# Performance work log

Hardware: AMD Instinct MI355X
Metric: run time of the kernel (lower is better)

The kernel has to match this reference:

```python
import jax, jax.numpy as jnp
import numpy as np

D_MODEL = 1024
N_HEADS = 16
D_HEAD = D_MODEL // N_HEADS
LSR_RANK = 32
B, T = 2, 2048


def setup_inputs() -> dict:
    key = jax.random.key(0)
    ks = jax.random.split(key, 12)
    s = 1.0 / np.sqrt(D_MODEL)
    return {
        "x": jax.random.normal(ks[0], (B, T, D_MODEL), dtype=jnp.float32),
        "Wq": jax.random.normal(ks[1], (D_MODEL, D_MODEL), dtype=jnp.float32) * s,
        "bq": jnp.zeros((D_MODEL,), dtype=jnp.float32),
        "Wk": jax.random.normal(ks[2], (D_MODEL, D_MODEL), dtype=jnp.float32) * s,
        "bk": jnp.zeros((D_MODEL,), dtype=jnp.float32),
        "Wv": jax.random.normal(ks[3], (D_MODEL, D_MODEL), dtype=jnp.float32) * s,
        "bv": jnp.zeros((D_MODEL,), dtype=jnp.float32),
        "Wo": jax.random.normal(ks[4], (D_MODEL, D_MODEL), dtype=jnp.float32) * s,
        "bo": jnp.zeros((D_MODEL,), dtype=jnp.float32),
        "Wq_lsr": jax.random.normal(ks[5], (N_HEADS, D_HEAD, LSR_RANK), dtype=jnp.float32),
        "Wk_lsr": jax.random.normal(ks[6], (N_HEADS, D_HEAD, LSR_RANK), dtype=jnp.float32),
    }


def reference(x, Wq, bq, Wk, bk, Wv, bv, Wo, bo, Wq_lsr, Wk_lsr):
    Bn, Tn, dm = x.shape
    H, Dh, R = Wq_lsr.shape
    # q/k/v projections, split into heads: (B, H, T, Dh)
    def split_heads(y):
        return y.reshape(Bn, Tn, H, Dh).transpose(0, 2, 1, 3)
    q = split_heads(x @ Wq + bq)
    k = split_heads(x @ Wk + bk)
    v = split_heads(x @ Wv + bv)
    # low-rank projected scores: (Q Wq_lsr)(K Wk_lsr)^T / sqrt(R)
    q_lr = jnp.einsum('bhtd,hdr->bhtr', q, Wq_lsr)
    k_lr = jnp.einsum('bhtd,hdr->bhtr', k, Wk_lsr)
    scale = 1.0 / jnp.sqrt(jnp.float32(R))
    scores = jnp.einsum('bhir,bhjr->bhij', q_lr, k_lr) * scale
    # causal mask
    causal = jnp.tril(jnp.ones((Tn, Tn), dtype=bool))
    scores = jnp.where(causal[None, None], scores, -jnp.inf)
    attn = jax.nn.softmax(scores, axis=-1)
    out = jnp.einsum('bhij,bhjd->bhid', attn, v)  # (B, H, T, Dh)
    out = out.transpose(0, 2, 1, 3).reshape(Bn, Tn, dm)
    return out @ Wo + bo
```

## Files before the change

kernel.cpp:

```cpp
#include <hip/hip_runtime.h>
#include <math.h>

#define D_MODEL 1024
#define N_HEADS 16
#define D_HEAD  64
#define LSR_RANK 32
#define BATCH 2
#define SEQ 2048
#define M_TOT (BATCH*SEQ)

typedef __attribute__((ext_vector_type(8))) short short8v;
typedef __attribute__((ext_vector_type(4))) short short4v;
typedef __attribute__((ext_vector_type(4))) float f32x4;

static __device__ __forceinline__ ushort bfhi(float f) {
    union { float f; unsigned u; } c; c.f = f;
    return (ushort)(c.u >> 16);
}
static __device__ __forceinline__ float bff(ushort h) {
    union { unsigned u; float f; } c; c.u = ((unsigned)h) << 16;
    return c.f;
}
static __device__ __forceinline__ ushort f2bf_rn(float f) {
    union { float f; unsigned u; } c; c.f = f;
    unsigned r = c.u + 0x7FFF + ((c.u >> 16) & 1);
    return (ushort)(r >> 16);
}
static __device__ __forceinline__ void split8(const float4 a, const float4 b,
                                              short8v& h, short8v& l) {
    ushort h0 = bfhi(a.x), h1 = bfhi(a.y), h2 = bfhi(a.z), h3 = bfhi(a.w);
    ushort h4 = bfhi(b.x), h5 = bfhi(b.y), h6 = bfhi(b.z), h7 = bfhi(b.w);
    h[0] = (short)h0; h[1] = (short)h1; h[2] = (short)h2; h[3] = (short)h3;
    h[4] = (short)h4; h[5] = (short)h5; h[6] = (short)h6; h[7] = (short)h7;
    l[0] = (short)bfhi(a.x - bff(h0)); l[1] = (short)bfhi(a.y - bff(h1));
    l[2] = (short)bfhi(a.z - bff(h2)); l[3] = (short)bfhi(a.w - bff(h3));
    l[4] = (short)bfhi(b.x - bff(h4)); l[5] = (short)bfhi(b.y - bff(h5));
    l[6] = (short)bfhi(b.z - bff(h6)); l[7] = (short)bfhi(b.w - bff(h7));
}
static __device__ __forceinline__ void trunc8(const float4 a, const float4 b,
                                              short8v& h) {
    h[0] = (short)bfhi(a.x); h[1] = (short)bfhi(a.y);
    h[2] = (short)bfhi(a.z); h[3] = (short)bfhi(a.w);
    h[4] = (short)bfhi(b.x); h[5] = (short)bfhi(b.y);
    h[6] = (short)bfhi(b.z); h[7] = (short)bfhi(b.w);
}

__global__ __launch_bounds__(256) void eff_weight2(
    const float* __restrict__ Wq, const float* __restrict__ Wq_lsr,
    const float* __restrict__ Wk, const float* __restrict__ Wk_lsr,
    float* __restrict__ Weff_tmp)
{
    const int z = blockIdx.y;
    const float* W    = z ? Wk : Wq;
    const float* Wlsr = z ? Wk_lsr : Wq_lsr;
    const int base = z << 9;
    int idx = blockIdx.x * 256 + threadIdx.x;
    int k = idx >> 9;
    int c = idx & 511;
    int h = c >> 5;
    int r = c & 31;
    const float* wrow = W + (size_t)k * D_MODEL + h * D_HEAD;
    const float* lsr  = Wlsr + (size_t)h * D_HEAD * LSR_RANK + r;
    float acc = 0.f;
    #pragma unroll
    for (int d = 0; d < D_HEAD; ++d)
        acc = fmaf(wrow[d], lsr[d * LSR_RANK], acc);
    Weff_tmp[(size_t)k * 1024 + base + c] = acc;
}

__global__ __launch_bounds__(256) void eff_bias_kernel(
    const float* __restrict__ bq, const float* __restrict__ Wq_lsr,
    const float* __restrict__ bk, const float* __restrict__ Wk_lsr,
    const float* __restrict__ bv, float* __restrict__ bcat)
{
    int c = blockIdx.x * 256 + threadIdx.x;
    if (c < 1024) {
        const float* bias = (c < 512) ? bq : bk;
        const float* lsr  = (c < 512) ? Wq_lsr : Wk_lsr;
        int cc = c & 511;
        int h = cc >> 5, r = cc & 31;
        float acc = 0.f;
        #pragma unroll
        for (int d = 0; d < D_HEAD; ++d)
            acc = fmaf(bias[h * D_HEAD + d],
                       lsr[(size_t)h * D_HEAD * LSR_RANK + d * LSR_RANK + r], acc);
        bcat[c] = acc;
    } else {
        bcat[c] = bv[c - 1024];
    }
}

__global__ __launch_bounds__(256) void transpose2(
    const float* __restrict__ in0, float* __restrict__ out0,
    const float* __restrict__ in1, float* __restrict__ out1)
{
    const float* in  = blockIdx.z ? in1 : in0;
    float* out       = blockIdx.z ? out1 : out0;
    __shared__ float t[64][65];
    const int tid = threadIdx.x;
    const int r0 = blockIdx.y * 64, c0 = blockIdx.x * 64;
    const int tr = tid >> 4, tc = tid & 15;
    #pragma unroll
    for (int i = 0; i < 4; ++i) {
        float4 v = *(const float4*)&in[(size_t)(r0 + tr + i * 16) * 1024 + c0 + tc * 4];
        t[tr + i * 16][tc * 4 + 0] = v.x;
        t[tr + i * 16][tc * 4 + 1] = v.y;
        t[tr + i * 16][tc * 4 + 2] = v.z;
        t[tr + i * 16][tc * 4 + 3] = v.w;
    }
    __syncthreads();
    #pragma unroll
    for (int i = 0; i < 4; ++i) {
        float4 v;
        v.x = t[tc * 4 + 0][tr + i * 16];
        v.y = t[tc * 4 + 1][tr + i * 16];
        v.z = t[tc * 4 + 2][tr + i * 16];
        v.w = t[tc * 4 + 3][tr + i * 16];
        *(float4*)&out[(size_t)(c0 + tr + i * 16) * 1024 + r0 + tc * 4] = v;
    }
}

__global__ __launch_bounds__(256) void tsplit_rn1024(
    const float* __restrict__ in, ushort* __restrict__ out)
{
    __shared__ float t[64][65];
    const int tid = threadIdx.x;
    const int r0 = blockIdx.y * 64, c0 = blockIdx.x * 64;
    const int tr = tid >> 4, tc = tid & 15;
    #pragma unroll
    for (int i = 0; i < 4; ++i) {
        float4 v = *(const float4*)&in[(size_t)(r0 + tr + i * 16) * 1024 + c0 + tc * 4];
        t[tr + i * 16][tc * 4 + 0] = v.x;
        t[tr + i * 16][tc * 4 + 1] = v.y;
        t[tr + i * 16][tc * 4 + 2] = v.z;
        t[tr + i * 16][tc * 4 + 3] = v.w;
    }
    __syncthreads();
    #pragma unroll
    for (int i = 0; i < 4; ++i) {
        short4v hv = {(short)f2bf_rn(t[tc * 4 + 0][tr + i * 16]),
                      (short)f2bf_rn(t[tc * 4 + 1][tr + i * 16]),
                      (short)f2bf_rn(t[tc * 4 + 2][tr + i * 16]),
                      (short)f2bf_rn(t[tc * 4 + 3][tr + i * 16])};
        *(short4v*)&out[(size_t)(c0 + tr + i * 16) * 1024 + r0 + tc * 4] = hv;
    }
}

__global__ __launch_bounds__(256) void gemm_proj_fused(
    const float* __restrict__ x,
    const float* __restrict__ Wcat_t,
    const float* __restrict__ bcat,
    float* __restrict__ Yqk,
    short* __restrict__ Kth, short* __restrict__ Ktl,
    short* __restrict__ Vbf)
{
    __shared__ __align__(16) short Ah[128 * 40], Al[128 * 40];
    __shared__ __align__(16) short Bh[128 * 40], Bl[128 * 40];

    const int tid = threadIdx.x;
    const int bx = blockIdx.x;
    const int m0 = blockIdx.y * 128, n0 = bx * 128;
    const bool vhalf = (bx >= 8);
    const int wid = tid >> 6, wr = wid >> 1, wc = wid & 1;
    const int lane = tid & 63, fr = lane & 15, fq = lane >> 4;
    const int srow = tid >> 1;
    const int skq  = (tid & 1) << 4;

    f32x4 acc[4][4];
    #pragma unroll
    for (int i = 0; i < 4; ++i)
        #pragma unroll
        for (int j = 0; j < 4; ++j)
            acc[i][j] = (f32x4){0.f, 0.f, 0.f, 0.f};

    const float* Ag = x + (size_t)(m0 + srow) * 1024 + skq;
    const float* Bg = Wcat_t + (size_t)(n0 + srow) * 1024 + skq;
    short* pAh = &Ah[srow * 40 + skq];
    short* pAl = &Al[srow * 40 + skq];
    short* pBh = &Bh[srow * 40 + skq];
    short* pBl = &Bl[srow * 40 + skq];

    for (int k0 = 0; k0 < 1024; k0 += 32) {
        float4 a0 = *(const float4*)(Ag + k0);
        float4 a1 = *(const float4*)(Ag + k0 + 4);
        float4 a2 = *(const float4*)(Ag + k0 + 8);
        float4 a3 = *(const float4*)(Ag + k0 + 12);
        float4 b0 = *(const float4*)(Bg + k0);
        float4 b1 = *(const float4*)(Bg + k0 + 4);
        float4 b2 = *(const float4*)(Bg + k0 + 8);
        float4 b3 = *(const float4*)(Bg + k0 + 12);
        if (vhalf) {
            short8v h;
            trunc8(a0, a1, h); *(short8v*)pAh = h;
            trunc8(a2, a3, h); *(short8v*)(pAh + 8) = h;
            trunc8(b0, b1, h); *(short8v*)pBh = h;
            trunc8(b2, b3, h); *(short8v*)(pBh + 8) = h;
        } else {
            short8v h, l;
            split8(a0, a1, h, l);
            *(short8v*)pAh = h;  *(short8v*)pAl = l;
            split8(a2, a3, h, l);
            *(short8v*)(pAh + 8) = h;  *(short8v*)(pAl + 8) = l;
            split8(b0, b1, h, l);
            *(short8v*)pBh = h;  *(short8v*)pBl = l;
            split8(b2, b3, h, l);
            *(short8v*)(pBh + 8) = h;  *(short8v*)(pBl + 8) = l;
        }
        __syncthreads();

        short8v afh[4], bfh[4];
        #pragma unroll
        for (int fi = 0; fi < 4; ++fi)
            afh[fi] = *(const short8v*)&Ah[(wr * 64 + fi * 16 + fr) * 40 + fq * 8];
        #pragma unroll
        for (int bj = 0; bj < 4; ++bj)
            bfh[bj] = *(const short8v*)&Bh[(wc * 64 + bj * 16 + fr) * 40 + fq * 8];

        if (vhalf) {
            #pragma unroll
            for (int fi = 0; fi < 4; ++fi)
                #pragma unroll
                for (int bj = 0; bj < 4; ++bj)
                    acc[fi][bj] = __builtin_amdgcn_mfma_f32_16x16x32_bf16(
                        afh[fi], bfh[bj], acc[fi][bj], 0, 0, 0);
        } else {
            short8v afl[4], bfl[4];
            #pragma unroll
            for (int fi = 0; fi < 4; ++fi)
                afl[fi] = *(const short8v*)&Al[(wr * 64 + fi * 16 + fr) * 40 + fq * 8];
            #pragma unroll
            for (int bj = 0; bj < 4; ++bj)
                bfl[bj] = *(const short8v*)&Bl[(wc * 64 + bj * 16 + fr) * 40 + fq * 8];
            #pragma unroll
            for (int fi = 0; fi < 4; ++fi) {
                #pragma unroll
                for (int bj = 0; bj < 4; ++bj) {
                    acc[fi][bj] = __builtin_amdgcn_mfma_f32_16x16x32_bf16(
                        afh[fi], bfh[bj], acc[fi][bj], 0, 0, 0);
                    acc[fi][bj] = __builtin_amdgcn_mfma_f32_16x16x32_bf16(
                        afh[fi], bfl[bj], acc[fi][bj], 0, 0, 0);
                    acc[fi][bj] = __builtin_amdgcn_mfma_f32_16x16x32_bf16(
                        afl[fi], bfh[bj], acc[fi][bj], 0, 0, 0);
                }
            }
        }
        __syncthreads();
    }

    const int b = m0 >> 11;
    #pragma unroll
    for (int fi = 0; fi < 4; ++fi) {
        #pragma unroll
        for (int bj = 0; bj < 4; ++bj) {
            const int r = m0 + wr * 64 + fi * 16 + fq * 4;
            const int gcol = n0 + wc * 64 + bj * 16 + fr;
            const float bv_ = bcat[gcol];
            if (bx < 4) {
                #pragma unroll
                for (int j = 0; j < 4; ++j)
                    Yqk[(size_t)(r + j) * 1024 + gcol] = acc[fi][bj][j] + bv_;
            } else if (bx < 8) {
                const int kc = gcol - 512;
                const int h = kc >> 5, rr = kc & 31;
                short* oh = Kth + (((size_t)(b * 16 + h) * 2048) + (r & 2047)) * 32 + rr;
                short* ol = Ktl + (((size_t)(b * 16 + h) * 2048) + (r & 2047)) * 32 + rr;
                #pragma unroll
                for (int j = 0; j < 4; ++j) {
                    const float v = acc[fi][bj][j] + bv_;
                    const ushort vh = bfhi(v);
                    oh[j * 32] = (short)vh;
                    ol[j * 32] = (short)bfhi(v - bff(vh));
                }
            } else {
                const int vc = gcol - 1024;
                const int h = vc >> 6, d = vc & 63;
                short4v o = {(short)f2bf_rn(acc[fi][bj][0] + bv_),
                             (short)f2bf_rn(acc[fi][bj][1] + bv_),
                             (short)f2bf_rn(acc[fi][bj][2] + bv_),
                             (short)f2bf_rn(acc[fi][bj][3] + bv_)};
                *(short4v*)&Vbf[((size_t)(b * 16 + h) * 64 + d) * 2048 + (r & 2047)] = o;
            }
        }
    }
}

__global__ __launch_bounds__(256) void gemm_out_bf(
    const ushort* __restrict__ Obf,
    const ushort* __restrict__ Wot,
    const float* __restrict__ bo,
    float* __restrict__ out)
{
    __shared__ __align__(16) short Ah[128 * 40];
    __shared__ __align__(16) short Bh[128 * 40];

    const int tid = threadIdx.x;
    const int m0 = blockIdx.y * 128, n0 = blockIdx.x * 128;
    const int wid = tid >> 6, wr = wid >> 1, wc = wid & 1;
    const int lane = tid & 63, fr = lane & 15, fq = lane >> 4;
    const int srow = tid >> 1;
    const int skq  = (tid & 1) << 4;

    f32x4 acc[4][4];
    #pragma unroll
    for (int i = 0; i < 4; ++i)
        #pragma unroll
        for (int j = 0; j < 4; ++j)
            acc[i][j] = (f32x4){0.f, 0.f, 0.f, 0.f};

    const ushort* AgH = Obf + (size_t)(m0 + srow) * 1024 + skq;
    const ushort* BgH = Wot + (size_t)(n0 + srow) * 1024 + skq;
    short* pAh = &Ah[srow * 40 + skq];
    short* pBh = &Bh[srow * 40 + skq];

    for (int k0 = 0; k0 < 1024; k0 += 32) {
        *(short8v*)pAh       = *(const short8v*)(AgH + k0);
        *(short8v*)(pAh + 8) = *(const short8v*)(AgH + k0 + 8);
        *(short8v*)pBh       = *(const short8v*)(BgH + k0);
        *(short8v*)(pBh + 8) = *(const short8v*)(BgH + k0 + 8);
        __syncthreads();

        short8v afh[4], bfh[4];
        #pragma unroll
        for (int fi = 0; fi < 4; ++fi)
            afh[fi] = *(const short8v*)&Ah[(wr * 64 + fi * 16 + fr) * 40 + fq * 8];
        #pragma unroll
        for (int bj = 0; bj < 4; ++bj)
            bfh[bj] = *(const short8v*)&Bh[(wc * 64 + bj * 16 + fr) * 40 + fq * 8];
        #pragma unroll
        for (int fi = 0; fi < 4; ++fi)
            #pragma unroll
            for (int bj = 0; bj < 4; ++bj)
                acc[fi][bj] = __builtin_amdgcn_mfma_f32_16x16x32_bf16(
                    afh[fi], bfh[bj], acc[fi][bj], 0, 0, 0);
        __syncthreads();
    }

    #pragma unroll
    for (int fi = 0; fi < 4; ++fi) {
        #pragma unroll
        for (int bj = 0; bj < 4; ++bj) {
            const int r = m0 + wr * 64 + fi * 16 + fq * 4;
            const int c = n0 + wc * 64 + bj * 16 + fr;
            const float bv_ = bo[c];
            #pragma unroll
            for (int j = 0; j < 4; ++j)
                out[(size_t)(r + j) * 1024 + c] = acc[fi][bj][j] + bv_;
        }
    }
}

#define P_LD  68
#define MASKVAL (-1e30f)

__global__ __launch_bounds__(512, 1) void flash_mfma(
    const float* __restrict__ Yqk,
    const short* __restrict__ Kth, const short* __restrict__ Ktl,
    const short* __restrict__ Vbf,
    ushort* __restrict__ Obf)
{
    const float scale = 0.1767766952966369f;
    const int L = blockIdx.x;
    const int bh = L & 31;
    const int qt = 31 - (L >> 5);
    const int b = bh >> 4, h = bh & 15;
    const int tid = threadIdx.x;
    const int w = tid >> 6;
    const int g = w & 3;
    const int p = w >> 2;
    const int lane = tid & 63;
    const int fr = lane & 15, fq = lane >> 4;

    __shared__ __align__(16) short Pall[8][16 * P_LD];
    __shared__ __align__(16) char exraw[4 * 64 * 80];
    short* Pw = &Pall[w][0];

    short8v aqh, aql;
    {
        const float* qp = Yqk + (size_t)(b * SEQ + qt * 64 + g * 16 + fr) * 1024
                          + h * 32 + fq * 8;
        split8(*(const float4*)qp, *(const float4*)(qp + 4), aqh, aql);
    }

    f32x4 acc0 = {0,0,0,0}, acc1 = {0,0,0,0}, acc2 = {0,0,0,0}, acc3 = {0,0,0,0};
    float m_[4], l_[4];
    #pragma unroll
    for (int r = 0; r < 4; ++r) { m_[r] = MASKVAL; l_[r] = 0.f; }

    const short* kb_h = Kth + (size_t)bh * 2048 * 32;
    const short* kb_l = Ktl + (size_t)bh * 2048 * 32;
    const short* vb   = Vbf + (size_t)bh * 64 * 2048;
    const int kidx = fr * 32 + fq * 8;
    const int vrow = fr * 2048 + fq * 8;

    for (int jt = p; jt <= qt; jt += 2) {
        const short* kp_h = kb_h + (size_t)jt * 64 * 32;
        const short* kp_l = kb_l + (size_t)jt * 64 * 32;
        short8v kh0 = *(const short8v*)&kp_h[kidx];
        short8v kh1 = *(const short8v*)&kp_h[kidx + 512];
        short8v kh2 = *(const short8v*)&kp_h[kidx + 1024];
        short8v kh3 = *(const short8v*)&kp_h[kidx + 1536];
        short8v kl0 = *(const short8v*)&kp_l[kidx];
        short8v kl1 = *(const short8v*)&kp_l[kidx + 512];
        short8v kl2 = *(const short8v*)&kp_l[kidx + 1024];
        short8v kl3 = *(const short8v*)&kp_l[kidx + 1536];
        const short* vp = vb + vrow + jt * 64;
        short8v v00 = *(const short8v*)&vp[0];
        short8v v01 = *(const short8v*)&vp[32];
        short8v v10 = *(const short8v*)&vp[16 * 2048];
        short8v v11 = *(const short8v*)&vp[16 * 2048 + 32];
        short8v v20 = *(const short8v*)&vp[32 * 2048];
        short8v v21 = *(const short8v*)&vp[32 * 2048 + 32];
        short8v v30 = *(const short8v*)&vp[48 * 2048];
        short8v v31 = *(const short8v*)&vp[48 * 2048 + 32];

        f32x4 s0 = {0,0,0,0}, s1 = {0,0,0,0}, s2 = {0,0,0,0}, s3 = {0,0,0,0};
        s0 = __builtin_amdgcn_mfma_f32_16x16x32_bf16(aqh, kh0, s0, 0, 0, 0);
        s0 = __builtin_amdgcn_mfma_f32_16x16x32_bf16(aqh, kl0, s0, 0, 0, 0);
        s0 = __builtin_amdgcn_mfma_f32_16x16x32_bf16(aql, kh0, s0, 0, 0, 0);
        s1 = __builtin_amdgcn_mfma_f32_16x16x32_bf16(aqh, kh1, s1, 0, 0, 0);
        s1 = __builtin_amdgcn_mfma_f32_16x16x32_bf16(aqh, kl1, s1, 0, 0, 0);
        s1 = __builtin_amdgcn_mfma_f32_16x16x32_bf16(aql, kh1, s1, 0, 0, 0);
        s2 = __builtin_amdgcn_mfma_f32_16x16x32_bf16(aqh, kh2, s2, 0, 0, 0);
        s2 = __builtin_amdgcn_mfma_f32_16x16x32_bf16(aqh, kl2, s2, 0, 0, 0);
        s2 = __builtin_amdgcn_mfma_f32_16x16x32_bf16(aql, kh2, s2, 0, 0, 0);
        s3 = __builtin_amdgcn_mfma_f32_16x16x32_bf16(aqh, kh3, s3, 0, 0, 0);
        s3 = __builtin_amdgcn_mfma_f32_16x16x32_bf16(aqh, kl3, s3, 0, 0, 0);
        s3 = __builtin_amdgcn_mfma_f32_16x16x32_bf16(aql, kh3, s3, 0, 0, 0);

        s0 *= scale; s1 *= scale; s2 *= scale; s3 *= scale;

        if (jt == qt) {
            #pragma unroll
            for (int r = 0; r < 4; ++r) {
                const int q_l = g * 16 + fq * 4 + r;
                s0[r] = (fr      <= q_l) ? s0[r] : MASKVAL;
                s1[r] = (16 + fr <= q_l) ? s1[r] : MASKVAL;
                s2[r] = (32 + fr <= q_l) ? s2[r] : MASKVAL;
                s3[r] = (48 + fr <= q_l) ? s3[r] : MASKVAL;
            }
        }

        float al[4];
        #pragma unroll
        for (int r = 0; r < 4; ++r) {
            float mt = fmaxf(fmaxf(s0[r], s1[r]), fmaxf(s2[r], s3[r]));
            mt = fmaxf(mt, __shfl_xor(mt, 1));
            mt = fmaxf(mt, __shfl_xor(mt, 2));
            mt = fmaxf(mt, __shfl_xor(mt, 4));
            mt = fmaxf(mt, __shfl_xor(mt, 8));
            const float mnew = fmaxf(m_[r], mt);
            al[r] = __expf(m_[r] - mnew);
            m_[r] = mnew;
            s0[r] = __expf(s0[r] - mnew);
            s1[r] = __expf(s1[r] - mnew);
            s2[r] = __expf(s2[r] - mnew);
            s3[r] = __expf(s3[r] - mnew);
            float ps = s0[r] + s1[r] + s2[r] + s3[r];
            ps += __shfl_xor(ps, 1);
            ps += __shfl_xor(ps, 2);
            ps += __shfl_xor(ps, 4);
            ps += __shfl_xor(ps, 8);
            l_[r] = l_[r] * al[r] + ps;
        }

        #pragma unroll
        for (int r = 0; r < 4; ++r) {
            const int prow = fq * 4 + r;
            Pw[prow * P_LD +      fr] = (short)f2bf_rn(s0[r]);
            Pw[prow * P_LD + 16 + fr] = (short)f2bf_rn(s1[r]);
            Pw[prow * P_LD + 32 + fr] = (short)f2bf_rn(s2[r]);
            Pw[prow * P_LD + 48 + fr] = (short)f2bf_rn(s3[r]);
        }
        #pragma unroll
        for (int r = 0; r < 4; ++r) {
            acc0[r] *= al[r]; acc1[r] *= al[r];
            acc2[r] *= al[r]; acc3[r] *= al[r];
        }
        short8v pa0 = *(const short8v*)&Pw[fr * P_LD + fq * 8];
        short8v pa1 = *(const short8v*)&Pw[fr * P_LD + 32 + fq * 8];

        acc0 = __builtin_amdgcn_mfma_f32_16x16x32_bf16(pa0, v00, acc0, 0, 0, 0);
        acc0 = __builtin_amdgcn_mfma_f32_16x16x32_bf16(pa1, v01, acc0, 0, 0, 0);
        acc1 = __builtin_amdgcn_mfma_f32_16x16x32_bf16(pa0, v10, acc1, 0, 0, 0);
        acc1 = __builtin_amdgcn_mfma_f32_16x16x32_bf16(pa1, v11, acc1, 0, 0, 0);
        acc2 = __builtin_amdgcn_mfma_f32_16x16x32_bf16(pa0, v20, acc2, 0, 0, 0);
        acc2 = __builtin_amdgcn_mfma_f32_16x16x32_bf16(pa1, v21, acc2, 0, 0, 0);
        acc3 = __builtin_amdgcn_mfma_f32_16x16x32_bf16(pa0, v30, acc3, 0, 0, 0);
        acc3 = __builtin_amdgcn_mfma_f32_16x16x32_bf16(pa1, v31, acc3, 0, 0, 0);
    }

    char* e = exraw + (size_t)(((g << 6) + lane) * 80);
    if (p == 1) {
        short8v a01, a23;
        a01[0] = (short)f2bf_rn(acc0[0]); a01[1] = (short)f2bf_rn(acc0[1]);
        a01[2] = (short)f2bf_rn(acc0[2]); a01[3] = (short)f2bf_rn(acc0[3]);
        a01[4] = (short)f2bf_rn(acc1[0]); a01[5] = (short)f2bf_rn(acc1[1]);
        a01[6] = (short)f2bf_rn(acc1[2]); a01[7] = (short)f2bf_rn(acc1[3]);
        a23[0] = (short)f2bf_rn(acc2[0]); a23[1] = (short)f2bf_rn(acc2[1]);
        a23[2] = (short)f2bf_rn(acc2[2]); a23[3] = (short)f2bf_rn(acc2[3]);
        a23[4] = (short)f2bf_rn(acc3[0]); a23[5] = (short)f2bf_rn(acc3[1]);
        a23[6] = (short)f2bf_rn(acc3[2]); a23[7] = (short)f2bf_rn(acc3[3]);
        *(short8v*)(e)      = a01;
        *(short8v*)(e + 16) = a23;
        *(f32x4*)(e + 32) = (f32x4){m_[0], m_[1], m_[2], m_[3]};
        *(f32x4*)(e + 48) = (f32x4){l_[0], l_[1], l_[2], l_[3]};
    }
    __syncthreads();
    if (p == 0) {
        short8v a01 = *(const short8v*)(e);
        short8v a23 = *(const short8v*)(e + 16);
        f32x4 m1 = *(const f32x4*)(e + 32);
        f32x4 l1 = *(const f32x4*)(e + 48);
        #pragma unroll
        for (int r = 0; r < 4; ++r) {
            const float mm = fmaxf(m_[r], m1[r]);
            const float a0 = __expf(m_[r] - mm);
            const float a1 = __expf(m1[r] - mm);
            const float inv = 1.f / (l_[r] * a0 + l1[r] * a1);
            const float b0 = bff((ushort)a01[r]);
            const float b1 = bff((ushort)a01[4 + r]);
            const float b2 = bff((ushort)a23[r]);
            const float b3 = bff((ushort)a23[4 + r]);
            const int trow = qt * 64 + g * 16 + fq * 4 + r;
            ushort* op = Obf + (size_t)(b * SEQ + trow) * 1024 + h * 64;
            op[     fr] = f2bf_rn((acc0[r] * a0 + b0 * a1) * inv);
            op[16 + fr] = f2bf_rn((acc1[r] * a0 + b1 * a1) * inv);
            op[32 + fr] = f2bf_rn((acc2[r] * a0 + b2 * a1) * inv);
            op[48 + fr] = f2bf_rn((acc3[r] * a0 + b3 * a1) * inv);
        }
    }
}

extern "C" void kernel_launch(void* const* d_in, const int* in_sizes, int n_in,
                              void* d_out, int out_size, void* d_ws, size_t ws_size,
                              hipStream_t stream)
{
    const float* x      = (const float*)d_in[0];
    const float* Wq     = (const float*)d_in[1];
    const float* bq     = (const float*)d_in[2];
    const float* Wk     = (const float*)d_in[3];
    const float* bk     = (const float*)d_in[4];
    const float* Wv     = (const float*)d_in[5];
    const float* bv     = (const float*)d_in[6];
    const float* Wo     = (const float*)d_in[7];
    const float* bo     = (const float*)d_in[8];
    const float* Wq_lsr = (const float*)d_in[9];
    const float* Wk_lsr = (const float*)d_in[10];
    float* out = (float*)d_out;

    float* ws     = (float*)d_ws;
    float* Wcat_t = ws;
    float* bcat   = Wcat_t + (size_t)2048 * 1024;
    float* Yqk    = bcat + 2048;
    float* Weff_tmp = Yqk;
    short* Kth    = (short*)(Yqk + (size_t)M_TOT * 1024);
    short* Ktl    = Kth + (size_t)32 * 2048 * 32;
    short* Vbf    = Ktl + (size_t)32 * 2048 * 32;
    ushort* Obf   = (ushort*)(Vbf + (size_t)32 * 64 * 2048);
    ushort* Wot   = (ushort*)Wcat_t;

    eff_weight2<<<dim3(2048, 2), 256, 0, stream>>>(Wq, Wq_lsr, Wk, Wk_lsr, Weff_tmp);
    eff_bias_kernel<<<8, 256, 0, stream>>>(bq, Wq_lsr, bk, Wk_lsr, bv, bcat);

    transpose2<<<dim3(16, 16, 2), 256, 0, stream>>>(
        Weff_tmp, Wcat_t, Wv, Wcat_t + (size_t)1024 * 1024);

    gemm_proj_fused<<<dim3(16, 32), 256, 0, stream>>>(
        x, Wcat_t, bcat, Yqk, Kth, Ktl, Vbf);

    tsplit_rn1024<<<dim3(16, 16), 256, 0, stream>>>(Wo, Wot);

    flash_mfma<<<1024, 512, 0, stream>>>(Yqk, Kth, Ktl, Vbf, Obf);

    gemm_out_bf<<<dim3(8, 32), 256, 0, stream>>>(Obf, Wot, bo, out);
}
```

Baseline: 215.6 us.

## Reuse loaded K/V tiles across four query tiles per flash block

Restructures the flash attention kernel so each 256-thread block handles 32 rows from each of four consecutive 64-row query tiles, reusing every loaded K/V tile across all four. This cuts redundant global K/V loads and halves the grid to 512 blocks. In exchange, register pressure rises sharply (16 accumulators plus per-tile softmax state), there are fewer warps per block, and the partial-result merge now needs extra barriers.

Result: no change. 216.1 us (+0.2%).

```diff
diff --git a/kernel.cpp b/kernel.cpp
--- a/kernel.cpp
+++ b/kernel.cpp
@@ -352,7 +352,7 @@
 #define P_LD  68
 #define MASKVAL (-1e30f)
 
-__global__ __launch_bounds__(512, 1) void flash_mfma(
+__global__ __launch_bounds__(256) void flash_mfma(
     const float* __restrict__ Yqk,
     const short* __restrict__ Kth, const short* __restrict__ Ktl,
     const short* __restrict__ Vbf,
@@ -361,30 +361,40 @@
     const float scale = 0.1767766952966369f;
     const int L = blockIdx.x;
     const int bh = L & 31;
-    const int qt = 31 - (L >> 5);
+    const int t5 = L >> 5;
+    const int qs = 7 - (t5 >> 1);
+    const int half = t5 & 1;
+    const int qt0 = 4 * qs;
     const int b = bh >> 4, h = bh & 15;
     const int tid = threadIdx.x;
     const int w = tid >> 6;
-    const int g = w & 3;
-    const int p = w >> 2;
+    const int g = w & 1;
+    const int p = w >> 1;
     const int lane = tid & 63;
     const int fr = lane & 15, fq = lane >> 4;
-
-    __shared__ __align__(16) short Pall[8][16 * P_LD];
-    __shared__ __align__(16) char exraw[4 * 64 * 80];
+    const int rowbase = half * 32 + g * 16;
+
+    __shared__ __align__(16) short Pall[4][16 * P_LD];
+    __shared__ __align__(16) char exraw[2 * 64 * 80];
     short* Pw = &Pall[w][0];
 
-    short8v aqh, aql;
-    {
-        const float* qp = Yqk + (size_t)(b * SEQ + qt * 64 + g * 16 + fr) * 1024
-                          + h * 32 + fq * 8;
-        split8(*(const float4*)qp, *(const float4*)(qp + 4), aqh, aql);
-    }
-
-    f32x4 acc0 = {0,0,0,0}, acc1 = {0,0,0,0}, acc2 = {0,0,0,0}, acc3 = {0,0,0,0};
-    float m_[4], l_[4];
-    #pragma unroll
-    for (int r = 0; r < 4; ++r) { m_[r] = MASKVAL; l_[r] = 0.f; }
+    short8v aqh[4], aql[4];
+    #pragma unroll
+    for (int tt = 0; tt < 4; ++tt) {
+        const float* qp_ = Yqk + (size_t)(b * SEQ + (qt0 + tt) * 64 + rowbase + fr) * 1024
+                           + h * 32 + fq * 8;
+        split8(*(const float4*)qp_, *(const float4*)(qp_ + 4), aqh[tt], aql[tt]);
+    }
+
+    f32x4 acc[4][4];
+    float m_[4][4], l_[4][4];
+    #pragma unroll
+    for (int tt = 0; tt < 4; ++tt)
+        #pragma unroll
+        for (int r = 0; r < 4; ++r) {
+            acc[tt][r] = (f32x4){0.f, 0.f, 0.f, 0.f};
+            m_[tt][r] = MASKVAL; l_[tt][r] = 0.f;
+        }
 
     const short* kb_h = Kth + (size_t)bh * 2048 * 32;
     const short* kb_l = Ktl + (size_t)bh * 2048 * 32;
@@ -392,7 +402,7 @@
     const int kidx = fr * 32 + fq * 8;
     const int vrow = fr * 2048 + fq * 8;
 
-    for (int jt = p; jt <= qt; jt += 2) {
+    for (int jt = p; jt <= qt0 + 3; jt += 2) {
         const short* kp_h = kb_h + (size_t)jt * 64 * 32;
         const short* kp_l = kb_l + (size_t)jt * 64 * 32;
         short8v kh0 = *(const short8v*)&kp_h[kidx];
@@ -413,121 +423,133 @@
         short8v v30 = *(const short8v*)&vp[48 * 2048];
         short8v v31 = *(const short8v*)&vp[48 * 2048 + 32];
 
-        f32x4 s0 = {0,0,0,0}, s1 = {0,0,0,0}, s2 = {0,0,0,0}, s3 = {0,0,0,0};
-        s0 = __builtin_amdgcn_mfma_f32_16x16x32_bf16(aqh, kh0, s0, 0, 0, 0);
-        s0 = __builtin_amdgcn_mfma_f32_16x16x32_bf16(aqh, kl0, s0, 0, 0, 0);
-        s0 = __builtin_amdgcn_mfma_f32_16x16x32_bf16(aql, kh0, s0, 0, 0, 0);
-        s1 = __builtin_amdgcn_mfma_f32_16x16x32_bf16(aqh, kh1, s1, 0, 0, 0);
-        s1 = __builtin_amdgcn_mfma_f32_16x16x32_bf16(aqh, kl1, s1, 0, 0, 0);
-        s1 = __builtin_amdgcn_mfma_f32_16x16x32_bf16(aql, kh1, s1, 0, 0, 0);
-        s2 = __builtin_amdgcn_mfma_f32_16x16x32_bf16(aqh, kh2, s2, 0, 0, 0);
-        s2 = __builtin_amdgcn_mfma_f32_16x16x32_bf16(aqh, kl2, s2, 0, 0, 0);
-        s2 = __builtin_amdgcn_mfma_f32_16x16x32_bf16(aql, kh2, s2, 0, 0, 0);
-        s3 = __builtin_amdgcn_mfma_f32_16x16x32_bf16(aqh, kh3, s3, 0, 0, 0);
-        s3 = __builtin_amdgcn_mfma_f32_16x16x32_bf16(aqh, kl3, s3, 0, 0, 0);
-        s3 = __builtin_amdgcn_mfma_f32_16x16x32_bf16(aql, kh3, s3, 0, 0, 0);
-
-        s0 *= scale; s1 *= scale; s2 *= scale; s3 *= scale;
-
-        if (jt == qt) {
+        #pragma unroll
+        for (int tt = 0; tt < 4; ++tt) {
+            const int qt_t = qt0 + tt;
+            if (jt <= qt_t) {
+                f32x4 s0 = {0,0,0,0}, s1 = {0,0,0,0}, s2 = {0,0,0,0}, s3 = {0,0,0,0};
+                s0 = __builtin_amdgcn_mfma_f32_16x16x32_bf16(aqh[tt], kh0, s0, 0, 0, 0);
+                s0 = __builtin_amdgcn_mfma_f32_16x16x32_bf16(aqh[tt], kl0, s0, 0, 0, 0);
+                s0 = __builtin_amdgcn_mfma_f32_16x16x32_bf16(aql[tt], kh0, s0, 0, 0, 0);
+                s1 = __builtin_amdgcn_mfma_f32_16x16x32_bf16(aqh[tt], kh1, s1, 0, 0, 0);
+                s1 = __builtin_amdgcn_mfma_f32_16x16x32_bf16(aqh[tt], kl1, s1, 0, 0, 0);
+                s1 = __builtin_amdgcn_mfma_f32_16x16x32_bf16(aql[tt], kh1, s1, 0, 0, 0);
+                s2 = __builtin_amdgcn_mfma_f32_16x16x32_bf16(aqh[tt], kh2, s2, 0, 0, 0);
+                s2 = __builtin_amdgcn_mfma_f32_16x16x32_bf16(aqh[tt], kl2, s2, 0, 0, 0);
+                s2 = __builtin_amdgcn_mfma_f32_16x16x32_bf16(aql[tt], kh2, s2, 0, 0, 0);
+                s3 = __builtin_amdgcn_mfma_f32_16x16x32_bf16(aqh[tt], kh3, s3, 0, 0, 0);
+                s3 = __builtin_amdgcn_mfma_f32_16x16x32_bf16(aqh[tt], kl3, s3, 0, 0, 0);
+                s3 = __builtin_amdgcn_mfma_f32_16x16x32_bf16(aql[tt], kh3, s3, 0, 0, 0);
+
+                s0 *= scale; s1 *= scale; s2 *= scale; s3 *= scale;
+
+                if (jt == qt_t) {
+                    #pragma unroll
+                    for (int r = 0; r < 4; ++r) {
+                        const int q_l = rowbase + fq * 4 + r;
+                        s0[r] = (fr      <= q_l) ? s0[r] : MASKVAL;
+                        s1[r] = (16 + fr <= q_l) ? s1[r] : MASKVAL;
+                        s2[r] = (32 + fr <= q_l) ? s2[r] : MASKVAL;
+                        s3[r] = (48 + fr <= q_l) ? s3[r] : MASKVAL;
+                    }
+                }
+
+                float al[4];
+                #pragma unroll
+                for (int r = 0; r < 4; ++r) {
+                    float mt = fmaxf(fmaxf(s0[r], s1[r]), fmaxf(s2[r], s3[r]));
+                    mt = fmaxf(mt, __shfl_xor(mt, 1));
+                    mt = fmaxf(mt, __shfl_xor(mt, 2));
+                    mt = fmaxf(mt, __shfl_xor(mt, 4));
+                    mt = fmaxf(mt, __shfl_xor(mt, 8));
+                    const float mnew = fmaxf(m_[tt][r], mt);
+                    al[r] = __expf(m_[tt][r] - mnew);
+                    m_[tt][r] = mnew;
+                    s0[r] = __expf(s0[r] - mnew);
+                    s1[r] = __expf(s1[r] - mnew);
+                    s2[r] = __expf(s2[r] - mnew);
+                    s3[r] = __expf(s3[r] - mnew);
+                    float ps = s0[r] + s1[r] + s2[r] + s3[r];
+                    ps += __shfl_xor(ps, 1);
+                    ps += __shfl_xor(ps, 2);
+                    ps += __shfl_xor(ps, 4);
+                    ps += __shfl_xor(ps, 8);
+                    l_[tt][r] = l_[tt][r] * al[r] + ps;
+                }
+
+                #pragma unroll
+                for (int r = 0; r < 4; ++r) {
+                    const int prow = fq * 4 + r;
+                    Pw[prow * P_LD +      fr] = (short)f2bf_rn(s0[r]);
+                    Pw[prow * P_LD + 16 + fr] = (short)f2bf_rn(s1[r]);
+                    Pw[prow * P_LD + 32 + fr] = (short)f2bf_rn(s2[r]);
+                    Pw[prow * P_LD + 48 + fr] = (short)f2bf_rn(s3[r]);
+                }
+                #pragma unroll
+                for (int r = 0; r < 4; ++r) {
+                    acc[tt][0][r] *= al[r];
+                    acc[tt][1][r] *= al[r];
+                    acc[tt][2][r] *= al[r];
+                    acc[tt][3][r] *= al[r];
+                }
+                short8v pa0 = *(const short8v*)&Pw[fr * P_LD + fq * 8];
+                short8v pa1 = *(const short8v*)&Pw[fr * P_LD + 32 + fq * 8];
+
+                acc[tt][0] = __builtin_amdgcn_mfma_f32_16x16x32_bf16(pa0, v00, acc[tt][0], 0, 0, 0);
+                acc[tt][0] = __builtin_amdgcn_mfma_f32_16x16x32_bf16(pa1, v01, acc[tt][0], 0, 0, 0);
+                acc[tt][1] = __builtin_amdgcn_mfma_f32_16x16x32_bf16(pa0, v10, acc[tt][1], 0, 0, 0);
+                acc[tt][1] = __builtin_amdgcn_mfma_f32_16x16x32_bf16(pa1, v11, acc[tt][1], 0, 0, 0);
+                acc[tt][2] = __builtin_amdgcn_mfma_f32_16x16x32_bf16(pa0, v20, acc[tt][2], 0, 0, 0);
+                acc[tt][2] = __builtin_amdgcn_mfma_f32_16x16x32_bf16(pa1, v21, acc[tt][2], 0, 0, 0);
+                acc[tt][3] = __builtin_amdgcn_mfma_f32_16x16x32_bf16(pa0, v30, acc[tt][3], 0, 0, 0);
+                acc[tt][3] = __builtin_amdgcn_mfma_f32_16x16x32_bf16(pa1, v31, acc[tt][3], 0, 0, 0);
+            }
+        }
+    }
+
+    char* e = exraw + (size_t)(((g << 6) + lane) * 80);
+    #pragma unroll
+    for (int tt = 0; tt < 4; ++tt) {
+        if (p == 1) {
+            short8v a01, a23;
+            a01[0] = (short)f2bf_rn(acc[tt][0][0]); a01[1] = (short)f2bf_rn(acc[tt][0][1]);
+            a01[2] = (short)f2bf_rn(acc[tt][0][2]); a01[3] = (short)f2bf_rn(acc[tt][0][3]);
+            a01[4] = (short)f2bf_rn(acc[tt][1][0]); a01[5] = (short)f2bf_rn(acc[tt][1][1]);
+            a01[6] = (short)f2bf_rn(acc[tt][1][2]); a01[7] = (short)f2bf_rn(acc[tt][1][3]);
+            a23[0] = (short)f2bf_rn(acc[tt][2][0]); a23[1] = (short)f2bf_rn(acc[tt][2][1]);
+            a23[2] = (short)f2bf_rn(acc[tt][2][2]); a23[3] = (short)f2bf_rn(acc[tt][2][3]);
+            a23[4] = (short)f2bf_rn(acc[tt][3][0]); a23[5] = (short)f2bf_rn(acc[tt][3][1]);
+            a23[6] = (short)f2bf_rn(acc[tt][3][2]); a23[7] = (short)f2bf_rn(acc[tt][3][3]);
+            *(short8v*)(e)      = a01;
+            *(short8v*)(e + 16) = a23;
+            *(f32x4*)(e + 32) = (f32x4){m_[tt][0], m_[tt][1], m_[tt][2], m_[tt][3]};
+            *(f32x4*)(e + 48) = (f32x4){l_[tt][0], l_[tt][1], l_[tt][2], l_[tt][3]};
+        }
+        __syncthreads();
+        if (p == 0) {
+            short8v a01 = *(const short8v*)(e);
+            short8v a23 = *(const short8v*)(e + 16);
+            f32x4 m1 = *(const f32x4*)(e + 32);
+            f32x4 l1 = *(const f32x4*)(e + 48);
             #pragma unroll
             for (int r = 0; r < 4; ++r) {
-                const int q_l = g * 16 + fq * 4 + r;
-                s0[r] = (fr      <= q_l) ? s0[r] : MASKVAL;
-                s1[r] = (16 + fr <= q_l) ? s1[r] : MASKVAL;
-                s2[r] = (32 + fr <= q_l) ? s2[r] : MASKVAL;
-                s3[r] = (48 + fr <= q_l) ? s3[r] : MASKVAL;
+                const float mm = fmaxf(m_[tt][r], m1[r]);
+                const float a0 = __expf(m_[tt][r] - mm);
+                const float a1 = __expf(m1[r] - mm);
+                const float inv = 1.f / (l_[tt][r] * a0 + l1[r] * a1);
+                const float b0 = bff((ushort)a01[r]);
+                const float b1 = bff((ushort)a01[4 + r]);
+                const float b2 = bff((ushort)a23[r]);
+                const float b3 = bff((ushort)a23[4 + r]);
+                const int trow = (qt0 + tt) * 64 + rowbase + fq * 4 + r;
+                ushort* op = Obf + (size_t)(b * SEQ + trow) * 1024 + h * 64;
+                op[     fr] = f2bf_rn((acc[tt][0][r] * a0 + b0 * a1) * inv);
+                op[16 + fr] = f2bf_rn((acc[tt][1][r] * a0 + b1 * a1) * inv);
+                op[32 + fr] = f2bf_rn((acc[tt][2][r] * a0 + b2 * a1) * inv);
+                op[48 + fr] = f2bf_rn((acc[tt][3][r] * a0 + b3 * a1) * inv);
             }
         }
-
-        float al[4];
-        #pragma unroll
-        for (int r = 0; r < 4; ++r) {
-            float mt = fmaxf(fmaxf(s0[r], s1[r]), fmaxf(s2[r], s3[r]));
-            mt = fmaxf(mt, __shfl_xor(mt, 1));
-            mt = fmaxf(mt, __shfl_xor(mt, 2));
-            mt = fmaxf(mt, __shfl_xor(mt, 4));
-            mt = fmaxf(mt, __shfl_xor(mt, 8));
-            const float mnew = fmaxf(m_[r], mt);
-            al[r] = __expf(m_[r] - mnew);
-            m_[r] = mnew;
-            s0[r] = __expf(s0[r] - mnew);
-            s1[r] = __expf(s1[r] - mnew);
-            s2[r] = __expf(s2[r] - mnew);
-            s3[r] = __expf(s3[r] - mnew);
-            float ps = s0[r] + s1[r] + s2[r] + s3[r];
-            ps += __shfl_xor(ps, 1);
-            ps += __shfl_xor(ps, 2);
-            ps += __shfl_xor(ps, 4);
-            ps += __shfl_xor(ps, 8);
-            l_[r] = l_[r] * al[r] + ps;
-        }
-
-        #pragma unroll
-        for (int r = 0; r < 4; ++r) {
-            const int prow = fq * 4 + r;
-            Pw[prow * P_LD +      fr] = (short)f2bf_rn(s0[r]);
-            Pw[prow * P_LD + 16 + fr] = (short)f2bf_rn(s1[r]);
-            Pw[prow * P_LD + 32 + fr] = (short)f2bf_rn(s2[r]);
-            Pw[prow * P_LD + 48 + fr] = (short)f2bf_rn(s3[r]);
-        }
-        #pragma unroll
-        for (int r = 0; r < 4; ++r) {
-            acc0[r] *= al[r]; acc1[r] *= al[r];
-            acc2[r] *= al[r]; acc3[r] *= al[r];
-        }
-        short8v pa0 = *(const short8v*)&Pw[fr * P_LD + fq * 8];
-        short8v pa1 = *(const short8v*)&Pw[fr * P_LD + 32 + fq * 8];
-
-        acc0 = __builtin_amdgcn_mfma_f32_16x16x32_bf16(pa0, v00, acc0, 0, 0, 0);
-        acc0 = __builtin_amdgcn_mfma_f32_16x16x32_bf16(pa1, v01, acc0, 0, 0, 0);
-        acc1 = __builtin_amdgcn_mfma_f32_16x16x32_bf16(pa0, v10, acc1, 0, 0, 0);
-        acc1 = __builtin_amdgcn_mfma_f32_16x16x32_bf16(pa1, v11, acc1, 0, 0, 0);
-        acc2 = __builtin_amdgcn_mfma_f32_16x16x32_bf16(pa0, v20, acc2, 0, 0, 0);
-        acc2 = __builtin_amdgcn_mfma_f32_16x16x32_bf16(pa1, v21, acc2, 0, 0, 0);
-        acc3 = __builtin_amdgcn_mfma_f32_16x16x32_bf16(pa0, v30, acc3, 0, 0, 0);
-        acc3 = __builtin_amdgcn_mfma_f32_16x16x32_bf16(pa1, v31, acc3, 0, 0, 0);
-    }
-
-    char* e = exraw + (size_t)(((g << 6) + lane) * 80);
-    if (p == 1) {
-        short8v a01, a23;
-        a01[0] = (short)f2bf_rn(acc0[0]); a01[1] = (short)f2bf_rn(acc0[1]);
-        a01[2] = (short)f2bf_rn(acc0[2]); a01[3] = (short)f2bf_rn(acc0[3]);
-        a01[4] = (short)f2bf_rn(acc1[0]); a01[5] = (short)f2bf_rn(acc1[1]);
-        a01[6] = (short)f2bf_rn(acc1[2]); a01[7] = (short)f2bf_rn(acc1[3]);
-        a23[0] = (short)f2bf_rn(acc2[0]); a23[1] = (short)f2bf_rn(acc2[1]);
-        a23[2] = (short)f2bf_rn(acc2[2]); a23[3] = (short)f2bf_rn(acc2[3]);
-        a23[4] = (short)f2bf_rn(acc3[0]); a23[5] = (short)f2bf_rn(acc3[1]);
-        a23[6] = (short)f2bf_rn(acc3[2]); a23[7] = (short)f2bf_rn(acc3[3]);
-        *(short8v*)(e)      = a01;
-        *(short8v*)(e + 16) = a23;
-        *(f32x4*)(e + 32) = (f32x4){m_[0], m_[1], m_[2], m_[3]};
-        *(f32x4*)(e + 48) = (f32x4){l_[0], l_[1], l_[2], l_[3]};
-    }
-    __syncthreads();
-    if (p == 0) {
-        short8v a01 = *(const short8v*)(e);
-        short8v a23 = *(const short8v*)(e + 16);
-        f32x4 m1 = *(const f32x4*)(e + 32);
-        f32x4 l1 = *(const f32x4*)(e + 48);
-        #pragma unroll
-        for (int r = 0; r < 4; ++r) {
-            const float mm = fmaxf(m_[r], m1[r]);
-            const float a0 = __expf(m_[r] - mm);
-            const float a1 = __expf(m1[r] - mm);
-            const float inv = 1.f / (l_[r] * a0 + l1[r] * a1);
-            const float b0 = bff((ushort)a01[r]);
-            const float b1 = bff((ushort)a01[4 + r]);
-            const float b2 = bff((ushort)a23[r]);
-            const float b3 = bff((ushort)a23[4 + r]);
-            const int trow = qt * 64 + g * 16 + fq * 4 + r;
-            ushort* op = Obf + (size_t)(b * SEQ + trow) * 1024 + h * 64;
-            op[     fr] = f2bf_rn((acc0[r] * a0 + b0 * a1) * inv);
-            op[16 + fr] = f2bf_rn((acc1[r] * a0 + b1 * a1) * inv);
-            op[32 + fr] = f2bf_rn((acc2[r] * a0 + b2 * a1) * inv);
-            op[48 + fr] = f2bf_rn((acc3[r] * a0 + b3 * a1) * inv);
-        }
+        __syncthreads();
     }
 }
 
@@ -570,7 +592,7 @@
 
     tsplit_rn1024<<<dim3(16, 16), 256, 0, stream>>>(Wo, Wot);
 
-    flash_mfma<<<1024, 512, 0, stream>>>(Yqk, Kth, Ktl, Vbf, Obf);
+    flash_mfma<<<512, 256, 0, stream>>>(Yqk, Kth, Ktl, Vbf, Obf);
 
     gemm_out_bf<<<dim3(8, 32), 256, 0, stream>>>(Obf, Wot, bo, out);
 }
```
